# Performance work log

Measured on AMD Instinct MI355X. Metric: run time of the kernel, lower is better.

Reference implementation:

```python
import jax, jax.numpy as jnp
import numpy as np

C = 256
EPS = 1e-5


def setup_inputs() -> dict:
    key = jax.random.key(0)
    ks = jax.random.split(key, 10)
    B, H, W = 4, 64, 64
    x1 = jax.random.normal(ks[0], (B, C, H, W), dtype=jnp.float32)
    x2 = jax.random.normal(ks[1], (B, C, H, W), dtype=jnp.float32)
    s = 1.0 / np.sqrt(C)
    qw = jax.random.normal(ks[2], (C, C), dtype=jnp.float32) * s
    qb = jax.random.normal(ks[3], (C,), dtype=jnp.float32) * 0.01
    kw = jax.random.normal(ks[4], (C, C), dtype=jnp.float32) * s
    kb = jax.random.normal(ks[5], (C,), dtype=jnp.float32) * 0.01
    vw = jax.random.normal(ks[6], (C, C), dtype=jnp.float32) * s
    vb = jax.random.normal(ks[7], (C,), dtype=jnp.float32) * 0.01
    ln_w = jnp.ones((C,), dtype=jnp.float32)
    ln_b = jnp.zeros((C,), dtype=jnp.float32)
    return {"x1": x1, "x2": x2, "qw": qw, "qb": qb, "kw": kw, "kb": kb,
            "vw": vw, "vb": vb, "ln_w": ln_w, "ln_b": ln_b}


def _conv1x1(x, w, b):
    # 1x1 conv == per-pixel matmul over channels. x: [B,C,H,W], w: [O,C]
    return jnp.einsum('oc,bchw->bohw', w, x) + b[None, :, None, None]


def reference(x1, x2, qw, qb, kw, kb, vw, vb, ln_w, ln_b):
    q = _conv1x1(x1, qw, qb)   # [B,C,H,W]
    k = _conv1x1(x2, kw, kb)   # [B,C,H,W]
    v = _conv1x1(x2, vw, vb)   # [B,C,H,W]
    # scores: [B,H,W,I,J]; softmax over LAST axis (j) only, as in the torch code
    scores = jnp.einsum('bchw,bcij->bhwij', q, k)
    attn = jax.nn.softmax(scores, axis=-1)
    fusion = jnp.einsum('bhwij,bcij->bchw', attn, v)  # [B,C,H,W]
    # LayerNorm2d: normalize over channel dim per spatial location
    mean = jnp.mean(fusion, axis=1, keepdims=True)
    var = jnp.var(fusion, axis=1, keepdims=True)
    normed = (fusion - mean) * jax.lax.rsqrt(var + EPS)
    return normed * ln_w[None, :, None, None] + ln_b[None, :, None, None]
```

## Files before the change

kernel.cpp:

```cpp
#include <hip/hip_runtime.h>


#define CDIM 256
#define NPOS 4096
#define BATCH 4
#define EPSV 1e-5f

typedef _Float16 f16;
typedef __attribute__((ext_vector_type(8))) _Float16 f16x8;
typedef __attribute__((ext_vector_type(4))) float f32x4;
typedef __attribute__((ext_vector_type(16))) float f32x16;

#define WST       264
#define QK_STRIDE 264
#define S_STRIDE  68
#define P_STRIDE  72
#define DQ_STRIDE 72
#define FT_STRIDE 66


static __device__ __forceinline__ f16x8 cvt8(const float* __restrict__ p) {
    float4 w0 = *(const float4*)p;
    float4 w1 = *(const float4*)(p + 4);
    f16x8 r;
    r[0] = (f16)w0.x; r[1] = (f16)w0.y; r[2] = (f16)w0.z; r[3] = (f16)w0.w;
    r[4] = (f16)w1.x; r[5] = (f16)w1.y; r[6] = (f16)w1.z; r[7] = (f16)w1.w;
    return r;
}

__global__ __launch_bounds__(256, 4) void prep_kernel(
    const float* __restrict__ x1, const float* __restrict__ x2,
    const float* __restrict__ qw, const float* __restrict__ kw,
    const float* __restrict__ vw,
    f16* __restrict__ X1T, f16* __restrict__ X2T, f16* __restrict__ W16)
{
    const int id = blockIdx.x;
    const int t  = threadIdx.x;
    if (id < 2048) {
        __shared__ f16 T[64 * 72];
        const float* xs = (id & 1) ? x2 : x1;
        f16* dst        = (id & 1) ? X2T : X1T;
        const int t2 = id >> 1;
        const int b  = t2 >> 8;
        const int rm = t2 & 255;
        const int c0 = (rm >> 6) * 64;
        const int n0 = (rm & 63) * 64;
        const float* src = xs + ((size_t)b * CDIM + c0) * NPOS + n0;
        const int rr = t >> 6, col = t & 63;
        #pragma unroll
        for (int j = 0; j < 16; ++j) {
            int row = rr + j * 4;
            T[col * 72 + row] = (f16)src[(size_t)row * NPOS + col];
        }
        __syncthreads();
        const int n = t >> 3, lc = (t & 7) * 8;
        f16* d0 = dst + ((size_t)b * NPOS + n0) * CDIM + c0;
        #pragma unroll
        for (int j = 0; j < 2; ++j) {
            int nn = n + j * 32;
            *(f16x8*)(d0 + (size_t)nn * CDIM + lc) = *(const f16x8*)&T[nn * 72 + lc];
        }
    } else {
        const int wblk = id - 2048;
        const int pr = wblk >> 2, h = wblk & 3;
        const float* W = (pr == 0 ? qw : pr == 1 ? kw : vw) + (size_t)h * 64 * CDIM;
        f16* D = W16 + (size_t)pr * CDIM * CDIM + (size_t)h * 64 * CDIM;
        #pragma unroll
        for (int i = 0; i < 8; ++i) {
            int g = t + i * 256;
            int row = g >> 5, col = (g & 31) * 8;
            *(f16x8*)(D + (size_t)row * CDIM + col) = cvt8(W + (size_t)row * CDIM + col);
        }
    }
}

__global__ __launch_bounds__(256, 2) void gemm_kernel(
    const f16* __restrict__ X1T, const f16* __restrict__ X2T,
    const f16* __restrict__ W16,
    const float* __restrict__ qb, const float* __restrict__ kb,
    const float* __restrict__ vb,
    f16* __restrict__ Qg, f16* __restrict__ Kg, f16* __restrict__ Vg)
{
    __shared__ f16 Xs[64 * WST];
    __shared__ f16 Wh[64 * WST];
    __shared__ f16 Ds[64 * DQ_STRIDE];
    __shared__ float biasS[256];

    const int id = blockIdx.x;
    const int pr  = id >> 8;
    const int rem = id & 255;
    const int b   = rem >> 6;
    const int p0  = (rem & 63) << 6;
    const f16* XT = (pr == 0) ? X1T : X2T;
    const f16* Wp = W16 + (size_t)pr * CDIM * CDIM;
    const float* bias = pr == 0 ? qb : pr == 1 ? kb : vb;

    const int t = threadIdx.x, w = t >> 6, l = t & 63, lm = l & 31, lh = l >> 5;
    const int pt = w & 1, ot = w >> 1;

    biasS[t] = bias[t];
    #pragma unroll
    for (int it = 0; it < 8; ++it) {
        int p = w * 16 + it * 2 + lh;
        *(f16x8*)&Xs[p * WST + lm * 8] =
            *(const f16x8*)(XT + ((size_t)(b * NPOS + p0 + p)) * CDIM + lm * 8);
    }

    for (int q = 0; q < 4; ++q) {
        #pragma unroll
        for (int i = 0; i < 8; ++i) {
            int g = t + i * 256;
            int row = g >> 5, col = (g & 31) * 8;
            *(f16x8*)&Wh[row * WST + col] =
                *(const f16x8*)(Wp + (size_t)(q * 64 + row) * CDIM + col);
        }
        __syncthreads();

        f32x16 accA = {}, accB = {};
        #pragma unroll
        for (int ks = 0; ks < 16; ks += 2) {
            f16x8 x0 = *(const f16x8*)&Xs[(pt * 32 + lm) * WST + ks * 16 + lh * 8];
            f16x8 w0 = *(const f16x8*)&Wh[(ot * 32 + lm) * WST + ks * 16 + lh * 8];
            f16x8 x1v = *(const f16x8*)&Xs[(pt * 32 + lm) * WST + (ks + 1) * 16 + lh * 8];
            f16x8 w1 = *(const f16x8*)&Wh[(ot * 32 + lm) * WST + (ks + 1) * 16 + lh * 8];
            if (pr < 2) {
                accA = __builtin_amdgcn_mfma_f32_32x32x16_f16(x0, w0, accA, 0, 0, 0);
                accB = __builtin_amdgcn_mfma_f32_32x32x16_f16(x1v, w1, accB, 0, 0, 0);
            } else {
                accA = __builtin_amdgcn_mfma_f32_32x32x16_f16(w0, x0, accA, 0, 0, 0);
                accB = __builtin_amdgcn_mfma_f32_32x32x16_f16(w1, x1v, accB, 0, 0, 0);
            }
        }

        if (pr < 2) {
            int o_l = ot * 32 + lm;
            float bv = biasS[q * 64 + o_l];
            #pragma unroll
            for (int r = 0; r < 16; ++r) {
                int p_l = pt * 32 + (r & 3) + 8 * (r >> 2) + 4 * lh;
                Ds[p_l * DQ_STRIDE + o_l] = (f16)(accA[r] + accB[r] + bv);
            }
        } else {
            #pragma unroll
            for (int r = 0; r < 16; ++r) {
                int o_l = ot * 32 + (r & 3) + 8 * (r >> 2) + 4 * lh;
                Ds[o_l * DQ_STRIDE + pt * 32 + lm] =
                    (f16)(accA[r] + accB[r] + biasS[q * 64 + o_l]);
            }
        }
        __syncthreads();

        #pragma unroll
        for (int j = 0; j < 2; ++j) {
            int row = (t >> 3) + j * 32;
            int cc  = (t & 7) * 8;
            f16x8 vdat = *(const f16x8*)&Ds[row * DQ_STRIDE + cc];
            if (pr < 2) {
                f16* Out = (pr == 0) ? Qg : Kg;
                *(f16x8*)(Out + ((size_t)(b * NPOS + p0 + row)) * CDIM + q * 64 + cc) = vdat;
            } else {
                *(f16x8*)(Vg + ((size_t)(b * CDIM + q * 64 + row)) * NPOS + p0 + cc) = vdat;
            }
        }
    }
}

__global__ __launch_bounds__(512, 1) void attn_kernel(
    const f16* __restrict__ Qg, const f16* __restrict__ Kg, const f16* __restrict__ Vg,
    const float* __restrict__ ln_w, const float* __restrict__ ln_b,
    float* __restrict__ out)
{
    __shared__ f16   Ks[2][64 * QK_STRIDE];
    __shared__ float Ss[2][64 * S_STRIDE];
    __shared__ f16   Ps[2][64 * P_STRIDE];
    __shared__ float lnw_s[256], lnb_s[256];
    __shared__ float redS[4 * 64], redQ[4 * 64], mu_s[64], rs_s[64];

    const int t   = threadIdx.x;
    const int b   = blockIdx.x >> 6;
    const int p0  = (blockIdx.x & 63) << 6;
    const int w   = t >> 6;
    const int g   = t >> 8;
    const int wl  = w & 3;
    const int tl  = t & 255;
    const int l   = t & 63;
    const int lm  = l & 31;
    const int lh  = l >> 5;

    if (t < 256) { lnw_s[t] = ln_w[t]; lnb_s[t] = ln_b[t]; }

    const int spt = wl & 1;
    const int skt = wl >> 1;

    f16x8 qf[16];
    {
        const f16* qptr = Qg + (size_t)(b * NPOS + p0 + spt * 32 + lm) * CDIM + lh * 8;
        #pragma unroll
        for (int ks = 0; ks < 16; ++ks) qf[ks] = *(const f16x8*)(qptr + ks * 16);
    }

    const int kr = tl >> 5, koff = (tl & 31) * 8;
    f16x8 kreg[8];
    auto issue_k = [&](int ch) {
        const int i0 = ch * 64;
        #pragma unroll
        for (int r = 0; r < 8; ++r)
            kreg[r] = *(const f16x8*)(Kg + (size_t)(b * NPOS + i0 + r * 8 + kr) * CDIM + koff);
    };
    issue_k(g);

    const f16* vbase0 = Vg + (size_t)(b * CDIM + wl * 64 + lm) * NPOS;
    const f16* vbase1 = Vg + (size_t)(b * CDIM + wl * 64 + 32 + lm) * NPOS;

    f32x16 facc[4] = {};

    for (int it = 0; it < 32; ++it) {
        const int ch = it * 2 + g;
        const int i0 = ch * 64;

        #pragma unroll
        for (int r = 0; r < 8; ++r)
            *(f16x8*)&Ks[g][(r * 8 + kr) * QK_STRIDE + koff] = kreg[r];
        __syncthreads();

        f16x8 vf0[4], vf1[4];
        #pragma unroll
        for (int ks = 0; ks < 4; ++ks) {
            vf0[ks] = *(const f16x8*)(vbase0 + i0 + ks * 16 + lh * 8);
            vf1[ks] = *(const f16x8*)(vbase1 + i0 + ks * 16 + lh * 8);
        }

        f32x16 sacc = {};
        #pragma unroll
        for (int ks = 0; ks < 16; ++ks) {
            f16x8 bb = *(const f16x8*)&Ks[g][(skt * 32 + lm) * QK_STRIDE + ks * 16 + lh * 8];
            sacc = __builtin_amdgcn_mfma_f32_32x32x16_f16(qf[ks], bb, sacc, 0, 0, 0);
        }
        #pragma unroll
        for (int r = 0; r < 16; ++r) {
            int row = (r & 3) + 8 * (r >> 2) + 4 * lh;
            Ss[g][(spt * 32 + row) * S_STRIDE + skt * 32 + lm] = sacc[r];
        }
        __syncthreads();

        {
            const int r  = tl >> 2;
            const int sg = (tl & 3) * 16;
            const float* srow = &Ss[g][r * S_STRIDE + sg];
            float v[16];
            f32x4 a0 = *(const f32x4*)(srow);
            f32x4 a1 = *(const f32x4*)(srow + 4);
            f32x4 a2 = *(const f32x4*)(srow + 8);
            f32x4 a3 = *(const f32x4*)(srow + 12);
            v[0]=a0[0]; v[1]=a0[1]; v[2]=a0[2]; v[3]=a0[3];
            v[4]=a1[0]; v[5]=a1[1]; v[6]=a1[2]; v[7]=a1[3];
            v[8]=a2[0]; v[9]=a2[1]; v[10]=a2[2]; v[11]=a2[3];
            v[12]=a3[0]; v[13]=a3[1]; v[14]=a3[2]; v[15]=a3[3];
            float m = v[0];
            #pragma unroll
            for (int i = 1; i < 16; ++i) m = fmaxf(m, v[i]);
            m = fmaxf(m, __shfl_xor(m, 1));
            m = fmaxf(m, __shfl_xor(m, 2));
            float s = 0.f;
            #pragma unroll
            for (int i = 0; i < 16; ++i) { float e = __expf(v[i] - m); v[i] = e; s += e; }
            s += __shfl_xor(s, 1);
            s += __shfl_xor(s, 2);
            float inv = __builtin_amdgcn_rcpf(s);
            f16x8 h0, h1;
            #pragma unroll
            for (int i = 0; i < 8; ++i) { h0[i] = (f16)(v[i] * inv); h1[i] = (f16)(v[i + 8] * inv); }
            *(f16x8*)&Ps[g][r * P_STRIDE + sg]     = h0;
            *(f16x8*)&Ps[g][r * P_STRIDE + sg + 8] = h1;
        }
        __syncthreads();

        if (it < 31) issue_k(ch + 2);

        #pragma unroll
        for (int ks = 0; ks < 4; ++ks) {
            f16x8 bp0 = *(const f16x8*)&Ps[g][lm * P_STRIDE + ks * 16 + lh * 8];
            f16x8 bp1 = *(const f16x8*)&Ps[g][(32 + lm) * P_STRIDE + ks * 16 + lh * 8];
            facc[0] = __builtin_amdgcn_mfma_f32_32x32x16_f16(vf0[ks], bp0, facc[0], 0, 0, 0);
            facc[1] = __builtin_amdgcn_mfma_f32_32x32x16_f16(vf0[ks], bp1, facc[1], 0, 0, 0);
            facc[2] = __builtin_amdgcn_mfma_f32_32x32x16_f16(vf1[ks], bp0, facc[2], 0, 0, 0);
            facc[3] = __builtin_amdgcn_mfma_f32_32x32x16_f16(vf1[ks], bp1, facc[3], 0, 0, 0);
        }
    }

    float* Ftmp = (float*)&Ks[0][0];
    __syncthreads();
    if (g == 1) {
        #pragma unroll
        for (int ii = 0; ii < 2; ++ii)
            #pragma unroll
            for (int jj = 0; jj < 2; ++jj)
                #pragma unroll
                for (int r = 0; r < 16; ++r) {
                    int c = wl * 64 + ii * 32 + (r & 3) + 8 * (r >> 2) + 4 * lh;
                    int p = jj * 32 + lm;
                    Ftmp[c * FT_STRIDE + p] = facc[ii * 2 + jj][r];
                }
    }
    __syncthreads();
    float ps0 = 0.f, ps1 = 0.f, pq0 = 0.f, pq1 = 0.f;
    if (g == 0) {
        #pragma unroll
        for (int ii = 0; ii < 2; ++ii)
            #pragma unroll
            for (int jj = 0; jj < 2; ++jj)
                #pragma unroll
                for (int r = 0; r < 16; ++r) {
                    int c = wl * 64 + ii * 32 + (r & 3) + 8 * (r >> 2) + 4 * lh;
                    int p = jj * 32 + lm;
                    facc[ii * 2 + jj][r] += Ftmp[c * FT_STRIDE + p];
                }
        #pragma unroll
        for (int ii = 0; ii < 2; ++ii) {
            #pragma unroll
            for (int r = 0; r < 16; ++r) {
                float a = facc[ii * 2 + 0][r];
                float c = facc[ii * 2 + 1][r];
                ps0 += a; pq0 += a * a;
                ps1 += c; pq1 += c * c;
            }
        }
        ps0 += __shfl_xor(ps0, 32); pq0 += __shfl_xor(pq0, 32);
        ps1 += __shfl_xor(ps1, 32); pq1 += __shfl_xor(pq1, 32);
        if (lh == 0) {
            redS[wl * 64 + lm] = ps0;        redQ[wl * 64 + lm] = pq0;
            redS[wl * 64 + 32 + lm] = ps1;   redQ[wl * 64 + 32 + lm] = pq1;
        }
    }
    __syncthreads();
    if (t < 64) {
        float s = redS[t] + redS[64 + t] + redS[128 + t] + redS[192 + t];
        float q = redQ[t] + redQ[64 + t] + redQ[128 + t] + redQ[192 + t];
        float mean = s * (1.0f / 256.0f);
        float var  = q * (1.0f / 256.0f) - mean * mean;
        mu_s[t] = mean;
        rs_s[t] = rsqrtf(var + EPSV);
    }
    __syncthreads();
    if (g == 0) {
        #pragma unroll
        for (int ii = 0; ii < 2; ++ii) {
            #pragma unroll
            for (int jj = 0; jj < 2; ++jj) {
                int p = jj * 32 + lm;
                float mu = mu_s[p], rs = rs_s[p];
                float* dst = out + (size_t)b * CDIM * NPOS + p0 + p;
                #pragma unroll
                for (int r = 0; r < 16; ++r) {
                    int c = wl * 64 + ii * 32 + (r & 3) + 8 * (r >> 2) + 4 * lh;
                    float vL = facc[ii * 2 + jj][r];
                    dst[(size_t)c * NPOS] = (vL - mu) * rs * lnw_s[c] + lnb_s[c];
                }
            }
        }
    }
}

extern "C" void kernel_launch(void* const* d_in, const int* in_sizes, int n_in,
                              void* d_out, int out_size, void* d_ws, size_t ws_size,
                              hipStream_t stream)
{
    const float* x1  = (const float*)d_in[0];
    const float* x2  = (const float*)d_in[1];
    const float* qw  = (const float*)d_in[2];
    const float* qb  = (const float*)d_in[3];
    const float* kw  = (const float*)d_in[4];
    const float* kb  = (const float*)d_in[5];
    const float* vw  = (const float*)d_in[6];
    const float* vb  = (const float*)d_in[7];
    const float* lnw = (const float*)d_in[8];
    const float* lnb = (const float*)d_in[9];

    const size_t tsz = (size_t)BATCH * NPOS * CDIM;
    f16* Qg  = (f16*)d_ws;
    f16* Kg  = Qg + tsz;
    f16* Vg  = Kg + tsz;
    f16* X1T = Vg + tsz;
    f16* X2T = X1T + tsz;
    f16* W16 = X2T + tsz;

    prep_kernel<<<2060, 256, 0, stream>>>(x1, x2, qw, kw, vw, X1T, X2T, W16);
    gemm_kernel<<<768, 256, 0, stream>>>(X1T, X2T, W16, qb, kb, vb, Qg, Kg, Vg);
    attn_kernel<<<256, 512, 0, stream>>>(Qg, Kg, Vg, lnw, lnb, (float*)d_out);
}
```

Measured before the change: 228.5 us.

## Split attention key range across four blocks and add separate merge+LayerNorm kernel

```diff
diff --git a/kernel.cpp b/kernel.cpp
--- a/kernel.cpp
+++ b/kernel.cpp
@@ -12,11 +12,10 @@
 typedef __attribute__((ext_vector_type(16))) float f32x16;
 
 #define WST       264
-#define QK_STRIDE 264
 #define S_STRIDE  68
 #define P_STRIDE  72
 #define DQ_STRIDE 72
-#define FT_STRIDE 66
+#define F_STRIDE  68
 
 
 static __device__ __forceinline__ f16x8 cvt8(const float* __restrict__ p) {
@@ -162,35 +161,28 @@
                 *(f16x8*)(Vg + ((size_t)(b * CDIM + q * 64 + row)) * NPOS + p0 + cc) = vdat;
             }
         }
-    }
-}
-
-__global__ __launch_bounds__(512, 1) void attn_kernel(
+        __syncthreads();
+    }
+}
+
+__global__ __launch_bounds__(256, 3) void attn_kernel(
     const f16* __restrict__ Qg, const f16* __restrict__ Kg, const f16* __restrict__ Vg,
-    const float* __restrict__ ln_w, const float* __restrict__ ln_b,
-    float* __restrict__ out)
-{
-    __shared__ f16   Ks[2][64 * QK_STRIDE];
-    __shared__ float Ss[2][64 * S_STRIDE];
-    __shared__ f16   Ps[2][64 * P_STRIDE];
-    __shared__ float lnw_s[256], lnb_s[256];
-    __shared__ float redS[4 * 64], redQ[4 * 64], mu_s[64], rs_s[64];
+    float* __restrict__ Fp)
+{
+    __shared__ float Ss[64 * S_STRIDE];
+    __shared__ f16   Ps[64 * P_STRIDE];
 
     const int t   = threadIdx.x;
-    const int b   = blockIdx.x >> 6;
-    const int p0  = (blockIdx.x & 63) << 6;
+    const int qtr = blockIdx.x & 3;
+    const int bq  = blockIdx.x >> 2;
+    const int b   = bq >> 6;
+    const int p0  = (bq & 63) << 6;
     const int w   = t >> 6;
-    const int g   = t >> 8;
-    const int wl  = w & 3;
-    const int tl  = t & 255;
     const int l   = t & 63;
     const int lm  = l & 31;
     const int lh  = l >> 5;
-
-    if (t < 256) { lnw_s[t] = ln_w[t]; lnb_s[t] = ln_b[t]; }
-
-    const int spt = wl & 1;
-    const int skt = wl >> 1;
+    const int spt = w & 1;
+    const int skt = w >> 1;
 
     f16x8 qf[16];
     {
@@ -199,54 +191,32 @@
         for (int ks = 0; ks < 16; ++ks) qf[ks] = *(const f16x8*)(qptr + ks * 16);
     }
 
-    const int kr = tl >> 5, koff = (tl & 31) * 8;
-    f16x8 kreg[8];
-    auto issue_k = [&](int ch) {
-        const int i0 = ch * 64;
-        #pragma unroll
-        for (int r = 0; r < 8; ++r)
-            kreg[r] = *(const f16x8*)(Kg + (size_t)(b * NPOS + i0 + r * 8 + kr) * CDIM + koff);
-    };
-    issue_k(g);
-
-    const f16* vbase0 = Vg + (size_t)(b * CDIM + wl * 64 + lm) * NPOS;
-    const f16* vbase1 = Vg + (size_t)(b * CDIM + wl * 64 + 32 + lm) * NPOS;
+    const f16* vb0 = Vg + (size_t)(b * CDIM + w * 64 + lm) * NPOS;
+    const f16* vb1 = Vg + (size_t)(b * CDIM + w * 64 + 32 + lm) * NPOS;
 
     f32x16 facc[4] = {};
 
-    for (int it = 0; it < 32; ++it) {
-        const int ch = it * 2 + g;
-        const int i0 = ch * 64;
-
-        #pragma unroll
-        for (int r = 0; r < 8; ++r)
-            *(f16x8*)&Ks[g][(r * 8 + kr) * QK_STRIDE + koff] = kreg[r];
-        __syncthreads();
-
-        f16x8 vf0[4], vf1[4];
-        #pragma unroll
-        for (int ks = 0; ks < 4; ++ks) {
-            vf0[ks] = *(const f16x8*)(vbase0 + i0 + ks * 16 + lh * 8);
-            vf1[ks] = *(const f16x8*)(vbase1 + i0 + ks * 16 + lh * 8);
-        }
-
+    for (int it = 0; it < 16; ++it) {
+        const int i0 = (qtr * 16 + it) * 64;
+
+        const f16* kp = Kg + (size_t)(b * NPOS + i0 + skt * 32 + lm) * CDIM + lh * 8;
         f32x16 sacc = {};
         #pragma unroll
         for (int ks = 0; ks < 16; ++ks) {
-            f16x8 bb = *(const f16x8*)&Ks[g][(skt * 32 + lm) * QK_STRIDE + ks * 16 + lh * 8];
+            f16x8 bb = *(const f16x8*)(kp + ks * 16);
             sacc = __builtin_amdgcn_mfma_f32_32x32x16_f16(qf[ks], bb, sacc, 0, 0, 0);
         }
         #pragma unroll
         for (int r = 0; r < 16; ++r) {
             int row = (r & 3) + 8 * (r >> 2) + 4 * lh;
-            Ss[g][(spt * 32 + row) * S_STRIDE + skt * 32 + lm] = sacc[r];
+            Ss[(spt * 32 + row) * S_STRIDE + skt * 32 + lm] = sacc[r];
         }
         __syncthreads();
 
         {
-            const int r  = tl >> 2;
-            const int sg = (tl & 3) * 16;
-            const float* srow = &Ss[g][r * S_STRIDE + sg];
+            const int r  = t >> 2;
+            const int sg = (t & 3) * 16;
+            const float* srow = &Ss[r * S_STRIDE + sg];
             float v[16];
             f32x4 a0 = *(const f32x4*)(srow);
             f32x4 a1 = *(const f32x4*)(srow + 4);
@@ -270,94 +240,93 @@
             f16x8 h0, h1;
             #pragma unroll
             for (int i = 0; i < 8; ++i) { h0[i] = (f16)(v[i] * inv); h1[i] = (f16)(v[i + 8] * inv); }
-            *(f16x8*)&Ps[g][r * P_STRIDE + sg]     = h0;
-            *(f16x8*)&Ps[g][r * P_STRIDE + sg + 8] = h1;
-        }
-        __syncthreads();
-
-        if (it < 31) issue_k(ch + 2);
+            *(f16x8*)&Ps[r * P_STRIDE + sg]     = h0;
+            *(f16x8*)&Ps[r * P_STRIDE + sg + 8] = h1;
+        }
+        __syncthreads();
 
         #pragma unroll
         for (int ks = 0; ks < 4; ++ks) {
-            f16x8 bp0 = *(const f16x8*)&Ps[g][lm * P_STRIDE + ks * 16 + lh * 8];
-            f16x8 bp1 = *(const f16x8*)&Ps[g][(32 + lm) * P_STRIDE + ks * 16 + lh * 8];
-            facc[0] = __builtin_amdgcn_mfma_f32_32x32x16_f16(vf0[ks], bp0, facc[0], 0, 0, 0);
-            facc[1] = __builtin_amdgcn_mfma_f32_32x32x16_f16(vf0[ks], bp1, facc[1], 0, 0, 0);
-            facc[2] = __builtin_amdgcn_mfma_f32_32x32x16_f16(vf1[ks], bp0, facc[2], 0, 0, 0);
-            facc[3] = __builtin_amdgcn_mfma_f32_32x32x16_f16(vf1[ks], bp1, facc[3], 0, 0, 0);
-        }
-    }
-
-    float* Ftmp = (float*)&Ks[0][0];
-    __syncthreads();
-    if (g == 1) {
-        #pragma unroll
-        for (int ii = 0; ii < 2; ++ii)
-            #pragma unroll
-            for (int jj = 0; jj < 2; ++jj)
-                #pragma unroll
-                for (int r = 0; r < 16; ++r) {
-                    int c = wl * 64 + ii * 32 + (r & 3) + 8 * (r >> 2) + 4 * lh;
-                    int p = jj * 32 + lm;
-                    Ftmp[c * FT_STRIDE + p] = facc[ii * 2 + jj][r];
-                }
-    }
-    __syncthreads();
-    float ps0 = 0.f, ps1 = 0.f, pq0 = 0.f, pq1 = 0.f;
-    if (g == 0) {
-        #pragma unroll
-        for (int ii = 0; ii < 2; ++ii)
-            #pragma unroll
-            for (int jj = 0; jj < 2; ++jj)
-                #pragma unroll
-                for (int r = 0; r < 16; ++r) {
-                    int c = wl * 64 + ii * 32 + (r & 3) + 8 * (r >> 2) + 4 * lh;
-                    int p = jj * 32 + lm;
-                    facc[ii * 2 + jj][r] += Ftmp[c * FT_STRIDE + p];
-                }
-        #pragma unroll
-        for (int ii = 0; ii < 2; ++ii) {
+            f16x8 av0 = *(const f16x8*)(vb0 + i0 + ks * 16 + lh * 8);
+            f16x8 av1 = *(const f16x8*)(vb1 + i0 + ks * 16 + lh * 8);
+            f16x8 bp0 = *(const f16x8*)&Ps[lm * P_STRIDE + ks * 16 + lh * 8];
+            f16x8 bp1 = *(const f16x8*)&Ps[(32 + lm) * P_STRIDE + ks * 16 + lh * 8];
+            facc[0] = __builtin_amdgcn_mfma_f32_32x32x16_f16(av0, bp0, facc[0], 0, 0, 0);
+            facc[1] = __builtin_amdgcn_mfma_f32_32x32x16_f16(av0, bp1, facc[1], 0, 0, 0);
+            facc[2] = __builtin_amdgcn_mfma_f32_32x32x16_f16(av1, bp0, facc[2], 0, 0, 0);
+            facc[3] = __builtin_amdgcn_mfma_f32_32x32x16_f16(av1, bp1, facc[3], 0, 0, 0);
+        }
+    }
+
+    float* dst = Fp + ((size_t)bq * 4 + qtr) * (CDIM * 64);
+    #pragma unroll
+    for (int ii = 0; ii < 2; ++ii)
+        #pragma unroll
+        for (int jj = 0; jj < 2; ++jj)
             #pragma unroll
             for (int r = 0; r < 16; ++r) {
-                float a = facc[ii * 2 + 0][r];
-                float c = facc[ii * 2 + 1][r];
-                ps0 += a; pq0 += a * a;
-                ps1 += c; pq1 += c * c;
-            }
-        }
-        ps0 += __shfl_xor(ps0, 32); pq0 += __shfl_xor(pq0, 32);
-        ps1 += __shfl_xor(ps1, 32); pq1 += __shfl_xor(pq1, 32);
-        if (lh == 0) {
-            redS[wl * 64 + lm] = ps0;        redQ[wl * 64 + lm] = pq0;
-            redS[wl * 64 + 32 + lm] = ps1;   redQ[wl * 64 + 32 + lm] = pq1;
-        }
+                int c = w * 64 + ii * 32 + (r & 3) + 8 * (r >> 2) + 4 * lh;
+                int p = jj * 32 + lm;
+                dst[c * 64 + p] = facc[ii * 2 + jj][r];
+            }
+}
+
+__global__ __launch_bounds__(256, 2) void merge_ln_kernel(
+    const float* __restrict__ Fp, const float* __restrict__ ln_w,
+    const float* __restrict__ ln_b, float* __restrict__ out)
+{
+    __shared__ float Fs[256 * F_STRIDE];
+    __shared__ float redS[16 * 64], redQ[16 * 64];
+    __shared__ float lnw_s[256], lnb_s[256];
+    __shared__ float mu_s[64], rs_s[64];
+
+    const int t  = threadIdx.x;
+    const int bq = blockIdx.x;
+    const int b  = bq >> 6;
+    const int p0 = (bq & 63) << 6;
+
+    lnw_s[t] = ln_w[t]; lnb_s[t] = ln_b[t];
+
+    const int pb = (t & 15) * 4;
+    const int cg = t >> 4;
+    const float* base = Fp + (size_t)bq * 4 * (CDIM * 64);
+
+    f32x4 s4 = {}, q4 = {};
+    #pragma unroll 4
+    for (int ci = 0; ci < 16; ++ci) {
+        int c = cg * 16 + ci;
+        size_t off = (size_t)c * 64 + pb;
+        f32x4 v = *(const f32x4*)(base + off);
+        v += *(const f32x4*)(base + (size_t)(CDIM * 64) + off);
+        v += *(const f32x4*)(base + (size_t)(2 * CDIM * 64) + off);
+        v += *(const f32x4*)(base + (size_t)(3 * CDIM * 64) + off);
+        *(f32x4*)&Fs[c * F_STRIDE + pb] = v;
+        s4 += v; q4 += v * v;
+    }
+    #pragma unroll
+    for (int k2 = 0; k2 < 4; ++k2) {
+        redS[cg * 64 + pb + k2] = s4[k2];
+        redQ[cg * 64 + pb + k2] = q4[k2];
     }
     __syncthreads();
     if (t < 64) {
-        float s = redS[t] + redS[64 + t] + redS[128 + t] + redS[192 + t];
-        float q = redQ[t] + redQ[64 + t] + redQ[128 + t] + redQ[192 + t];
-        float mean = s * (1.0f / 256.0f);
-        float var  = q * (1.0f / 256.0f) - mean * mean;
+        float ss = 0.f, qq = 0.f;
+        #pragma unroll
+        for (int g2 = 0; g2 < 16; ++g2) { ss += redS[g2 * 64 + t]; qq += redQ[g2 * 64 + t]; }
+        float mean = ss * (1.0f / 256.0f);
+        float var  = qq * (1.0f / 256.0f) - mean * mean;
         mu_s[t] = mean;
         rs_s[t] = rsqrtf(var + EPSV);
     }
     __syncthreads();
-    if (g == 0) {
-        #pragma unroll
-        for (int ii = 0; ii < 2; ++ii) {
-            #pragma unroll
-            for (int jj = 0; jj < 2; ++jj) {
-                int p = jj * 32 + lm;
-                float mu = mu_s[p], rs = rs_s[p];
-                float* dst = out + (size_t)b * CDIM * NPOS + p0 + p;
-                #pragma unroll
-                for (int r = 0; r < 16; ++r) {
-                    int c = wl * 64 + ii * 32 + (r & 3) + 8 * (r >> 2) + 4 * lh;
-                    float vL = facc[ii * 2 + jj][r];
-                    dst[(size_t)c * NPOS] = (vL - mu) * rs * lnw_s[c] + lnb_s[c];
-                }
-            }
-        }
+    const int p   = t & 63;
+    const int cg2 = t >> 6;
+    const float mu = mu_s[p], rs = rs_s[p];
+    float* dst = out + (size_t)b * CDIM * NPOS + p0 + p;
+    #pragma unroll 4
+    for (int ci = 0; ci < 64; ++ci) {
+        int c = cg2 * 64 + ci;
+        dst[(size_t)c * NPOS] = (Fs[c * F_STRIDE + p] - mu) * rs * lnw_s[c] + lnb_s[c];
     }
 }
 
@@ -383,8 +352,10 @@
     f16* X1T = Vg + tsz;
     f16* X2T = X1T + tsz;
     f16* W16 = X2T + tsz;
+    float* Fp = (float*)X1T;
 
     prep_kernel<<<2060, 256, 0, stream>>>(x1, x2, qw, kw, vw, X1T, X2T, W16);
     gemm_kernel<<<768, 256, 0, stream>>>(X1T, X2T, W16, qb, kb, vb, Qg, Kg, Vg);
-    attn_kernel<<<256, 512, 0, stream>>>(Qg, Kg, Vg, lnw, lnb, (float*)d_out);
-}
+    attn_kernel<<<1024, 256, 0, stream>>>(Qg, Kg, Vg, Fp);
+    merge_ln_kernel<<<256, 256, 0, stream>>>(Fp, lnw, lnb, (float*)d_out);
+}
```

Result: slower. 352.2 us (+54.1%).
